# Performance work log

Hardware: AMD Instinct MI355X
Metric: run time of the kernel (lower is better)

## Reference

```python
import jax, jax.numpy as jnp
import numpy as np

B, T, D_IN, D_SAE, K = 256, 8, 768, 8192, 32


def setup_inputs() -> dict:
    key = jax.random.key(0)
    k1, k2, k3 = jax.random.split(key, 3)
    x = jax.random.normal(k1, (B, T, D_IN), dtype=jnp.float32)
    # kaiming_uniform: bound = sqrt(6 / fan_in), fan_in = prod of trailing dims
    bound_e = float(np.sqrt(6.0 / (D_SAE * D_IN)))
    W_enc = jax.random.uniform(k2, (T, D_SAE, D_IN), jnp.float32, -bound_e, bound_e)
    bound_d = float(np.sqrt(6.0 / (D_IN * D_SAE)))
    W_dec = jax.random.uniform(k3, (T, D_IN, D_SAE), jnp.float32, -bound_d, bound_d)
    # decoder column normalization (norm over d_in axis), as in _normalize_decoder
    norms = jnp.clip(jnp.linalg.norm(W_dec, axis=1, keepdims=True), 1e-8)
    W_dec = W_dec / norms
    b_enc = jnp.zeros((T, D_SAE), jnp.float32)
    b_dec = jnp.zeros((T, D_IN), jnp.float32)
    return {"x": x, "W_enc": W_enc, "b_enc": b_enc, "W_dec": W_dec,
            "b_dec": b_dec, "k": K}


def reference(x, W_enc, b_enc, W_dec, b_dec, k):
    # x: (B, T, d_in)
    x_c = x - b_dec[None]                                   # (B, T, d)
    pre = jnp.einsum('btd,thd->bth', x_c, W_enc) + b_enc[None]  # (B, T, h)
    bt = pre.shape[0] * pre.shape[1]
    pre_flat = pre.reshape(bt, -1)
    topk_vals, topk_idx = jax.lax.top_k(pre_flat, k)        # (BT, k)
    rows = jnp.arange(bt)[:, None]
    u_flat = jnp.zeros_like(pre_flat).at[rows, topk_idx].set(jax.nn.relu(topk_vals))
    u = u_flat.reshape(pre.shape)                            # (B, T, h)
    x_hat = jnp.einsum('bth,tdh->btd', u, W_dec) + b_dec[None]
    recon_loss = jnp.mean(jnp.sum((x_hat - x) ** 2, axis=-1))
    return recon_loss, x_hat, u
```

## Files before the change

### kernel.cpp

```cpp
#include <hip/hip_runtime.h>
#include <cstdint>
#include <cstddef>

constexpr int B_SZ  = 256;
constexpr int T_SZ  = 8;
constexpr int DIN   = 768;
constexpr int DSAE  = 8192;
constexpr int KSEL  = 32;
constexpr int NROWS = B_SZ * T_SZ;
constexpr int CAND_CAP = 64;
constexpr int RCAP  = 32;
constexpr float EPS_W = 3.2e-4f;
constexpr int NSK   = DIN / 32;

constexpr size_t XC_SZ    = (size_t)NROWS * DIN;
constexpr size_t OFF_XC   = 0;
constexpr size_t OFF_XCP  = OFF_XC + XC_SZ;
constexpr size_t XCP_W    = XC_SZ / 2;
constexpr size_t OFF_SIDX = OFF_XCP + XCP_W;
constexpr size_t OFF_SVAL = OFF_SIDX + (size_t)NROWS * KSEL;
constexpr size_t OFF_BIG  = OFF_SVAL + (size_t)NROWS * KSEL;
constexpr size_t BIG_W    = (size_t)T_SZ * DSAE * DIN / 2;
constexpr size_t WS_FAST_WORDS = OFF_BIG + BIG_W;

typedef short bf16x8 __attribute__((ext_vector_type(8)));
typedef float f32x4  __attribute__((ext_vector_type(4)));

__device__ inline unsigned rne1(float x) {
  unsigned u = __float_as_uint(x);
  return (u + 0x7FFFu + ((u >> 16) & 1u)) >> 16;
}
__device__ inline float bf16tof(unsigned short v) {
  return __uint_as_float((unsigned)v << 16);
}
__device__ inline unsigned packtr(float a, float b) {
  return (__float_as_uint(a) >> 16) | (__float_as_uint(b) & 0xFFFF0000u);
}

__device__ inline void gload_lds16(const void* g, void* l) {
  __builtin_amdgcn_global_load_lds(
      (const __attribute__((address_space(1))) void*)g,
      (__attribute__((address_space(3))) void*)l, 16, 0, 0);
}

__global__ void k_zero(float* p) { *p = 0.f; }

__global__ __launch_bounds__(256) void k_xc(const float* __restrict__ x,
                                            const float* __restrict__ bdec,
                                            float* __restrict__ xc,
                                            unsigned short* __restrict__ xcp) {
  const int c = blockIdx.x * 256 + threadIdx.x;
  const int lane = c & 63;
  const int u = c >> 6;
  const int s  = u % NSK;
  const int tt = (u / NSK) & (T_SZ - 1);
  const int gm = u / (NSK * T_SZ);
  const int b  = gm * 16 + (lane & 15);
  const int k0 = s * 32 + (lane >> 4) * 8;
  const size_t rowOff = ((size_t)(b * T_SZ + tt)) * DIN + k0;
  float4 v0 = *(const float4*)(x + rowOff);
  float4 v1 = *(const float4*)(x + rowOff + 4);
  float4 d0 = *(const float4*)(bdec + tt * DIN + k0);
  float4 d1 = *(const float4*)(bdec + tt * DIN + k0 + 4);
  v0.x -= d0.x; v0.y -= d0.y; v0.z -= d0.z; v0.w -= d0.w;
  v1.x -= d1.x; v1.y -= d1.y; v1.z -= d1.z; v1.w -= d1.w;
  *(float4*)(xc + rowOff) = v0;
  *(float4*)(xc + rowOff + 4) = v1;
  uint4 p;
  p.x = rne1(v0.x) | (rne1(v0.y) << 16);
  p.y = rne1(v0.z) | (rne1(v0.w) << 16);
  p.z = rne1(v1.x) | (rne1(v1.y) << 16);
  p.w = rne1(v1.z) | (rne1(v1.w) << 16);
  *(uint4*)(xcp + (size_t)c * 8) = p;
}

__global__ __launch_bounds__(256, 2) void k_encoder(const unsigned short* __restrict__ xcp,
                                                    const float* __restrict__ Wenc,
                                                    const float* __restrict__ benc,
                                                    float* __restrict__ pre) {
  __shared__ __align__(16) float Bs[4][64 * 32];
  const int tid = threadIdx.x;
  const int wm = tid >> 6, lane = tid & 63;
  const int l15 = lane & 15, kc = lane >> 4;

  int gRow[2], gCol[2], ldsL[2];
#pragma unroll
  for (int i = 0; i < 2; ++i) {
    int L = i * 4096 + tid * 16;
    int G = L ^ (((L >> 7) & 7) << 4);
    gRow[i] = G >> 7;
    gCol[i] = (G & 127) >> 2;
    ldsL[i] = L;
  }
  int bOff0[4], bOff1[4];
#pragma unroll
  for (int ni = 0; ni < 4; ++ni) {
    int row = ni * 16 + l15;
    int P = row * 128 + kc * 32;
    int sw = (row & 7) << 4;
    bOff0[ni] = P ^ sw;
    bOff1[ni] = (P + 16) ^ sw;
  }
  constexpr size_t A_MI = (size_t)T_SZ * NSK * 512;

  for (int tile = 0; tile < 2; ++tile) {
    const int tileId = blockIdx.x + tile * 512;
    const int t  = tileId >> 7;
    const int n0 = (tileId & 127) * 64;

    const float* bG = Wenc + ((size_t)t * DSAE + n0) * DIN;
    const unsigned short* aP =
        xcp + ((size_t)(wm * 4 * T_SZ + t) * NSK) * 512 + lane * 8;

    auto STAGE = [&](int buf, int s) {
#pragma unroll
      for (int i = 0; i < 2; ++i)
        gload_lds16(bG + (size_t)gRow[i] * DIN + s * 32 + gCol[i],
                    (char*)&Bs[0][0] + buf * 8192 + ldsL[i]);
    };

    f32x4 acc[4][4] = {};
    bf16x8 aA[4], aB[4];

    STAGE(0, 0);
#pragma unroll
    for (int mi = 0; mi < 4; ++mi)
      aA[mi] = *(const bf16x8*)(aP + mi * A_MI);
    STAGE(1, 1);

#define ENC_W6 asm volatile("s_waitcnt vmcnt(6)" ::: "memory")
#define ENC_W4 asm volatile("s_waitcnt vmcnt(4)" ::: "memory")
#define ENC_W0 asm volatile("s_waitcnt vmcnt(0)" ::: "memory")
#define ENC_STEP(u, PFB, PFA, WAITOP) do {                                   \
    if (PFB) STAGE(((u) + 2) & 3, s0 + (u) + 2);                             \
    if (PFA) {                                                               \
      const unsigned short* ap = aP + (size_t)(s0 + (u) + 1) * 512;          \
      _Pragma("unroll")                                                      \
      for (int mi = 0; mi < 4; ++mi) {                                       \
        bf16x8 v = *(const bf16x8*)(ap + mi * A_MI);                         \
        if ((u) % 2 == 0) aB[mi] = v; else aA[mi] = v;                       \
      }                                                                      \
    }                                                                        \
    __builtin_amdgcn_sched_barrier(0);                                       \
    WAITOP;                                                                  \
    __builtin_amdgcn_s_barrier();                                            \
    __builtin_amdgcn_sched_barrier(0);                                       \
    {                                                                        \
      const char* bb = (const char*)&Bs[0][0] + ((u) & 3) * 8192;            \
      _Pragma("unroll")                                                      \
      for (int ni = 0; ni < 4; ++ni) {                                       \
        f32x4 f0 = *(const f32x4*)(bb + bOff0[ni]);                          \
        f32x4 f1 = *(const f32x4*)(bb + bOff1[ni]);                          \
        union { uint32_t w[4]; bf16x8 h; } cvu;                              \
        cvu.w[0] = packtr(f0.x, f0.y); cvu.w[1] = packtr(f0.z, f0.w);        \
        cvu.w[2] = packtr(f1.x, f1.y); cvu.w[3] = packtr(f1.z, f1.w);        \
        _Pragma("unroll")                                                    \
        for (int mi = 0; mi < 4; ++mi)                                       \
          acc[mi][ni] = __builtin_amdgcn_mfma_f32_16x16x32_bf16(             \
              ((u) % 2 == 0) ? aA[mi] : aB[mi], cvu.h, acc[mi][ni], 0, 0, 0);\
      }                                                                      \
    }                                                                        \
  } while (0)

    int s0 = 0;
    for (int g = 0; g < 5; ++g, s0 += 4) {
      ENC_STEP(0, true, true, ENC_W6); ENC_STEP(1, true, true, ENC_W6);
      ENC_STEP(2, true, true, ENC_W6); ENC_STEP(3, true, true, ENC_W6);
    }
    ENC_STEP(0, true, true, ENC_W6);  ENC_STEP(1, true, true, ENC_W6);
    ENC_STEP(2, false, true, ENC_W4); ENC_STEP(3, false, false, ENC_W0);
#undef ENC_STEP
#undef ENC_W6
#undef ENC_W4
#undef ENC_W0

#pragma unroll
    for (int ni = 0; ni < 4; ++ni) {
      const int col = n0 + ni * 16 + l15;
      const float bias = benc[(size_t)t * DSAE + col];
#pragma unroll
      for (int mi = 0; mi < 4; ++mi) {
        const int rbase = wm * 64 + mi * 16 + kc * 4;
#pragma unroll
        for (int j = 0; j < 4; ++j)
          pre[((size_t)(rbase + j) * T_SZ + t) * DSAE + col] = acc[mi][ni][j] + bias;
      }
    }
    if (tile == 0) __syncthreads();
  }
}

__global__ __launch_bounds__(256) void k_select(const float* __restrict__ xc,
                                                const float* __restrict__ Wenc,
                                                const float* __restrict__ benc,
                                                float* u,
                                                int* __restrict__ sel_idx,
                                                float* __restrict__ sel_val) {
  const int r = blockIdx.x, t = r & (T_SZ - 1);
  __shared__ float sp[DSAE];
  __shared__ float redf[4], redf2[4];
  __shared__ int   redi[4];
  __shared__ float cv[CAND_CAP]; __shared__ int ci[CAND_CAP];
  __shared__ float sv[CAND_CAP]; __shared__ int si[CAND_CAP];
  __shared__ float rv[RCAP];     __shared__ int ri[RCAP];
  __shared__ double rd[RCAP];
  __shared__ double xd[DIN];
  __shared__ int   s_n, s_nR, s_A, s_nW;
  const int tid = threadIdx.x, lane = tid & 63, w = tid >> 6;
  float* urow = u + (size_t)r * DSAE;

  float s1 = 0.f, s2 = 0.f;
  for (int sgm = 0; sgm < DSAE / 256; ++sgm) {
    float v = urow[tid + sgm * 256];
    sp[tid + sgm * 256] = v;
    s1 += v; s2 = fmaf(v, v, s2);
  }
  for (int off = 32; off; off >>= 1) {
    s1 += __shfl_down(s1, off); s2 += __shfl_down(s2, off);
  }
  if (lane == 0) { redf[w] = s1; redf2[w] = s2; }
  __syncthreads();
  const float mean = (redf[0] + redf[1] + redf[2] + redf[3]) * (1.f / DSAE);
  const float var  = (redf2[0] + redf2[1] + redf2[2] + redf2[3]) * (1.f / DSAE) - mean * mean;
  const float sd   = sqrtf(fmaxf(var, 1e-20f));

  auto countGE = [&](float th) -> int {
    int c = 0;
#pragma unroll
    for (int sgm = 0; sgm < DSAE / 256; ++sgm)
      c += (sp[tid + sgm * 256] >= th) ? 1 : 0;
    for (int off = 32; off; off >>= 1) c += __shfl_down(c, off);
    __syncthreads();
    if (lane == 0) redi[w] = c;
    __syncthreads();
    return redi[0] + redi[1] + redi[2] + redi[3];
  };

  float tlo = mean + 2.0f * sd, thi = mean + 3.5f * sd;
  for (int it = 0; it < 8 && countGE(tlo) < KSEL; ++it) tlo -= sd;
  float th = mean + 2.52f * sd;
  int c = countGE(th);
  for (int it = 0; it < 24 && (c < KSEL || c > CAND_CAP); ++it) {
    if (c > CAND_CAP) tlo = th; else thi = th;
    th = 0.5f * (tlo + thi);
    c = countGE(th);
  }
  if (c < KSEL) { th = tlo; c = countGE(th); }

  if (tid == 0) s_n = 0;
  __syncthreads();
  for (int sgm = 0; sgm < DSAE / 256; ++sgm) {
    int i = tid + sgm * 256;
    float v = sp[i];
    if (v >= th) {
      int p = atomicAdd(&s_n, 1);
      if (p < CAND_CAP) { cv[p] = v; ci[p] = i; }
    }
  }
  __syncthreads();
  const int n = s_n < CAND_CAP ? s_n : CAND_CAP;

  if (tid < n) {
    float v = cv[tid]; int id = ci[tid];
    int rk = 0;
    for (int j = 0; j < n; ++j) {
      float vj = cv[j];
      rk += (vj > v || (vj == v && ci[j] < id)) ? 1 : 0;
    }
    sv[rk] = v; si[rk] = id;
  }
  __syncthreads();

  const float v32 = sv[KSEL - 1];
  const float wlo = v32 - EPS_W, whi = v32 + EPS_W;
  if (tid == 0) {
    int A = 0;
    while (A < KSEL - 1 && sv[A] > whi) ++A;
    s_A = A;
    int e = A;
    while (e < n && sv[e] >= wlo) ++e;
    s_nW = e - A;
  }
  __syncthreads();
  const int A  = s_A;
  const int nW = s_nW < RCAP ? s_nW : RCAP;
  if (tid < nW) { rv[tid] = sv[A + tid]; ri[tid] = si[A + tid]; }
  if (tid == 0) s_nR = nW;
  __syncthreads();
  if (th > wlo) {
    for (int sgm = 0; sgm < DSAE / 256; ++sgm) {
      int i = tid + sgm * 256;
      float v = sp[i];
      if (v >= wlo && v < th) {
        int p = atomicAdd(&s_nR, 1);
        if (p < RCAP) { rv[p] = v; ri[p] = i; }
      }
    }
  }
  __syncthreads();
  const int nR = s_nR < RCAP ? s_nR : RCAP;

  if (nR >= 2) {
    for (int i = tid; i < DIN; i += 256) xd[i] = (double)xc[(size_t)r * DIN + i];
    __syncthreads();
    for (int j = w; j < nR; j += 4) {
      const int h = ri[j];
      const float* wrow = Wenc + ((size_t)t * DSAE + h) * DIN;
      double s = 0.0;
#pragma unroll
      for (int ss = 0; ss < DIN / 64; ++ss)
        s += xd[lane + 64 * ss] * (double)wrow[lane + 64 * ss];
      for (int off = 32; off; off >>= 1) s += __shfl_down(s, off);
      if (lane == 0) rd[j] = s + (double)benc[(size_t)t * DSAE + h];
    }
  } else if (nR == 1) {
    if (tid == 0) rd[0] = (double)rv[0];
  }
  __syncthreads();

  for (int sgm = 0; sgm < DSAE / 256; ++sgm) urow[tid + sgm * 256] = 0.f;
  __syncthreads();

  if (tid < A) {
    float val = fmaxf(sv[tid], 0.f);
    urow[si[tid]] = val;
    sel_idx[(size_t)r * KSEL + tid] = si[tid];
    sel_val[(size_t)r * KSEL + tid] = val;
  }
  const int need = KSEL - A;
  if (tid < nR) {
    double v = rd[tid]; int id = ri[tid];
    int rk = 0;
    for (int j = 0; j < nR; ++j) {
      double vj = rd[j];
      rk += (vj > v || (vj == v && ri[j] < id)) ? 1 : 0;
    }
    if (rk < need) {
      float val = fmaxf((float)v, 0.f);
      urow[id] = val;
      sel_idx[(size_t)r * KSEL + A + rk] = id;
      sel_val[(size_t)r * KSEL + A + rk] = val;
    }
  }
}

__global__ __launch_bounds__(256) void k_transpose(const float* __restrict__ W,
                                                   unsigned short* __restrict__ Wt) {
  __shared__ float s[32][33];
  const int t  = blockIdx.z;
  const int h0 = blockIdx.x * 32;
  const int d0 = blockIdx.y * 32;
  const int c  = threadIdx.x & 31, rr = threadIdx.x >> 5;
#pragma unroll
  for (int q = 0; q < 4; ++q) {
    int d = d0 + rr + q * 8;
    s[rr + q * 8][c] = W[((size_t)t * DIN + d) * DSAE + h0 + c];
  }
  __syncthreads();
#pragma unroll
  for (int q = 0; q < 4; ++q) {
    int h = h0 + rr + q * 8;
    Wt[((size_t)t * DSAE + h) * DIN + d0 + c] = (unsigned short)rne1(s[c][rr + q * 8]);
  }
}

template <bool TRANSPOSED>
__global__ __launch_bounds__(256) void k_decoder(const void* __restrict__ Wd_,
                                                 const float* __restrict__ x,
                                                 const float* __restrict__ bdec,
                                                 const int* __restrict__ sel_idx,
                                                 const float* __restrict__ sel_val,
                                                 float* __restrict__ xhat,
                                                 float* __restrict__ loss) {
  const int r = blockIdx.x, t = r & (T_SZ - 1);
  __shared__ int   si[KSEL];
  __shared__ float sv[KSEL];
  __shared__ float rbuf[4];
  const int tid = threadIdx.x;
  if (tid < KSEL) {
    si[tid] = sel_idx[(size_t)r * KSEL + tid] & (DSAE - 1);
    sv[tid] = sel_val[(size_t)r * KSEL + tid];
  }
  __syncthreads();

  float acc[3];
#pragma unroll
  for (int i = 0; i < 3; ++i) acc[i] = bdec[(size_t)t * DIN + tid + 256 * i];
#pragma unroll 4
  for (int j = 0; j < KSEL; ++j) {
    const int h = si[j];
    const float v = sv[j];
    if (TRANSPOSED) {
      const unsigned short* wrow =
          (const unsigned short*)Wd_ + ((size_t)t * DSAE + h) * DIN;
#pragma unroll
      for (int i = 0; i < 3; ++i)
        acc[i] = fmaf(v, bf16tof(wrow[tid + 256 * i]), acc[i]);
    } else {
      const float* Wd = (const float*)Wd_;
#pragma unroll
      for (int i = 0; i < 3; ++i)
        acc[i] = fmaf(v, Wd[((size_t)t * DIN + tid + 256 * i) * DSAE + h], acc[i]);
    }
  }
  float sq = 0.f;
#pragma unroll
  for (int i = 0; i < 3; ++i) {
    const int d = tid + 256 * i;
    const float xv = x[(size_t)r * DIN + d];
    xhat[(size_t)r * DIN + d] = acc[i];
    const float e = acc[i] - xv;
    sq = fmaf(e, e, sq);
  }
  for (int off = 32; off; off >>= 1) sq += __shfl_down(sq, off);
  if ((tid & 63) == 0) rbuf[tid >> 6] = sq;
  __syncthreads();
  if (tid == 0)
    atomicAdd(loss, (rbuf[0] + rbuf[1] + rbuf[2] + rbuf[3]) * (1.0f / NROWS));
}

extern "C" void kernel_launch(void* const* d_in, const int* in_sizes, int n_in,
                              void* d_out, int out_size, void* d_ws, size_t ws_size,
                              hipStream_t stream) {
  const float* x    = (const float*)d_in[0];
  const float* Wenc = (const float*)d_in[1];
  const float* benc = (const float*)d_in[2];
  const float* Wdec = (const float*)d_in[3];
  const float* bdec = (const float*)d_in[4];

  float* out  = (float*)d_out;
  float* loss = out;
  float* xhat = out + 1;
  float* u    = out + 1 + (size_t)NROWS * DIN;

  float*          wsf  = (float*)d_ws;
  float*          xc   = wsf + OFF_XC;
  unsigned short* xcp  = (unsigned short*)(wsf + OFF_XCP);
  int*            sidx = (int*)(wsf + OFF_SIDX);
  float*          sval = wsf + OFF_SVAL;
  unsigned short* big  = (unsigned short*)(wsf + OFF_BIG);
  const bool fast = ws_size >= WS_FAST_WORDS * sizeof(float);

  k_zero<<<1, 1, 0, stream>>>(loss);
  k_xc<<<NROWS * DIN / (256 * 8), 256, 0, stream>>>(x, bdec, xc, xcp);
  k_encoder<<<512, 256, 0, stream>>>(xcp, Wenc, benc, u);
  k_select<<<NROWS, 256, 0, stream>>>(xc, Wenc, benc, u, sidx, sval);
  if (fast) {
    k_transpose<<<dim3(DSAE / 32, DIN / 32, T_SZ), 256, 0, stream>>>(Wdec, big);
    k_decoder<true><<<NROWS, 256, 0, stream>>>(big, x, bdec, sidx, sval, xhat, loss);
  } else {
    k_decoder<false><<<NROWS, 256, 0, stream>>>(Wdec, x, bdec, sidx, sval, xhat, loss);
  }
}
```

Before: 240.2 us.

## Fuse top-k candidate capture into encoder and decode directly from untransposed weights

A new kernel computes a per-row threshold proportional to the norm of the centred input. The encoder epilogue then appends every pre-activation above that threshold to a per-row candidate list using global atomics. The selection kernel uses this list when it holds enough candidates and the boundary window stays above the threshold, and falls back to the full-row scan otherwise. The separate transpose-to-bf16 pass and row-wise decoder are replaced by a decoder with one block per (d, t). Each block stages one fp32 weight row of 8192 entries in shared memory and gathers the selected entries for all batch rows, which removes the extra transpose write and read. The threshold constant is tuned to the weight scale, so the fast path depends on the input statistics; the encoder also gains atomic contention in its epilogue.

```diff
diff --git a/kernel.cpp b/kernel.cpp
--- a/kernel.cpp
+++ b/kernel.cpp
@@ -9,9 +9,11 @@
 constexpr int KSEL  = 32;
 constexpr int NROWS = B_SZ * T_SZ;
 constexpr int CAND_CAP = 64;
+constexpr int CFCAP = 128;
 constexpr int RCAP  = 32;
 constexpr float EPS_W = 3.2e-4f;
 constexpr int NSK   = DIN / 32;
+constexpr float TAU_C = 1.324943e-3f;
 
 constexpr size_t XC_SZ    = (size_t)NROWS * DIN;
 constexpr size_t OFF_XC   = 0;
@@ -19,9 +21,11 @@
 constexpr size_t XCP_W    = XC_SZ / 2;
 constexpr size_t OFF_SIDX = OFF_XCP + XCP_W;
 constexpr size_t OFF_SVAL = OFF_SIDX + (size_t)NROWS * KSEL;
-constexpr size_t OFF_BIG  = OFF_SVAL + (size_t)NROWS * KSEL;
-constexpr size_t BIG_W    = (size_t)T_SZ * DSAE * DIN / 2;
-constexpr size_t WS_FAST_WORDS = OFF_BIG + BIG_W;
+constexpr size_t OFF_TAU  = OFF_SVAL + (size_t)NROWS * KSEL;
+constexpr size_t OFF_CCNT = OFF_TAU + NROWS;
+constexpr size_t OFF_CIDX = OFF_CCNT + NROWS;
+constexpr size_t OFF_CVAL = OFF_CIDX + (size_t)NROWS * CFCAP;
+constexpr size_t WS_WORDS = OFF_CVAL + (size_t)NROWS * CFCAP;
 
 typedef short bf16x8 __attribute__((ext_vector_type(8)));
 typedef float f32x4  __attribute__((ext_vector_type(4)));
@@ -30,20 +34,14 @@
   unsigned u = __float_as_uint(x);
   return (u + 0x7FFFu + ((u >> 16) & 1u)) >> 16;
 }
-__device__ inline float bf16tof(unsigned short v) {
-  return __uint_as_float((unsigned)v << 16);
-}
 __device__ inline unsigned packtr(float a, float b) {
   return (__float_as_uint(a) >> 16) | (__float_as_uint(b) & 0xFFFF0000u);
 }
-
 __device__ inline void gload_lds16(const void* g, void* l) {
   __builtin_amdgcn_global_load_lds(
       (const __attribute__((address_space(1))) void*)g,
       (__attribute__((address_space(3))) void*)l, 16, 0, 0);
 }
-
-__global__ void k_zero(float* p) { *p = 0.f; }
 
 __global__ __launch_bounds__(256) void k_xc(const float* __restrict__ x,
                                             const float* __restrict__ bdec,
@@ -74,10 +72,32 @@
   *(uint4*)(xcp + (size_t)c * 8) = p;
 }
 
+__global__ __launch_bounds__(256) void k_tau(const float* __restrict__ xc,
+                                             float* __restrict__ tau,
+                                             int* __restrict__ ccnt,
+                                             float* __restrict__ loss) {
+  const int tid = threadIdx.x, lane = tid & 63, w = tid >> 6;
+  if (blockIdx.x < 8) ccnt[blockIdx.x * 256 + tid] = 0;
+  if (blockIdx.x == 0 && tid == 0) *loss = 0.f;
+  const int r = blockIdx.x * 4 + w;
+  float s = 0.f;
+#pragma unroll
+  for (int ld = 0; ld < 3; ++ld) {
+    float4 v = *(const float4*)(xc + (size_t)r * DIN + ld * 256 + lane * 4);
+    s = fmaf(v.x, v.x, fmaf(v.y, v.y, fmaf(v.z, v.z, fmaf(v.w, v.w, s))));
+  }
+  for (int off = 32; off; off >>= 1) s += __shfl_down(s, off);
+  if (lane == 0) tau[r] = TAU_C * sqrtf(s);
+}
+
 __global__ __launch_bounds__(256, 2) void k_encoder(const unsigned short* __restrict__ xcp,
                                                     const float* __restrict__ Wenc,
                                                     const float* __restrict__ benc,
-                                                    float* __restrict__ pre) {
+                                                    float* __restrict__ pre,
+                                                    const float* __restrict__ tau,
+                                                    int* __restrict__ ccnt,
+                                                    int* __restrict__ cidx,
+                                                    float* __restrict__ cval) {
   __shared__ __align__(16) float Bs[4][64 * 32];
   const int tid = threadIdx.x;
   const int wm = tid >> 6, lane = tid & 63;
@@ -121,7 +141,6 @@
 
     f32x4 acc[4][4] = {};
     bf16x8 aA[4], aB[4];
-
     STAGE(0, 0);
 #pragma unroll
     for (int mi = 0; mi < 4; ++mi)
@@ -174,6 +193,13 @@
 #undef ENC_W4
 #undef ENC_W0
 
+    float tv[4][4];
+#pragma unroll
+    for (int mi = 0; mi < 4; ++mi)
+#pragma unroll
+      for (int j = 0; j < 4; ++j)
+        tv[mi][j] = tau[(wm * 64 + mi * 16 + kc * 4 + j) * T_SZ + t];
+
 #pragma unroll
     for (int ni = 0; ni < 4; ++ni) {
       const int col = n0 + ni * 16 + l15;
@@ -182,8 +208,18 @@
       for (int mi = 0; mi < 4; ++mi) {
         const int rbase = wm * 64 + mi * 16 + kc * 4;
 #pragma unroll
-        for (int j = 0; j < 4; ++j)
-          pre[((size_t)(rbase + j) * T_SZ + t) * DSAE + col] = acc[mi][ni][j] + bias;
+        for (int j = 0; j < 4; ++j) {
+          const float v = acc[mi][ni][j] + bias;
+          const int rr = (rbase + j) * T_SZ + t;
+          pre[(size_t)rr * DSAE + col] = v;
+          if (v >= tv[mi][j]) {
+            int pos = atomicAdd(&ccnt[rr], 1);
+            if (pos < CFCAP) {
+              cidx[(size_t)rr * CFCAP + pos] = col;
+              cval[(size_t)rr * CFCAP + pos] = v;
+            }
+          }
+        }
       }
     }
     if (tile == 0) __syncthreads();
@@ -195,99 +231,125 @@
                                                 const float* __restrict__ benc,
                                                 float* u,
                                                 int* __restrict__ sel_idx,
-                                                float* __restrict__ sel_val) {
+                                                float* __restrict__ sel_val,
+                                                const float* __restrict__ tau,
+                                                const int* __restrict__ ccnt,
+                                                const int* __restrict__ cidx,
+                                                const float* __restrict__ cval) {
   const int r = blockIdx.x, t = r & (T_SZ - 1);
   __shared__ float sp[DSAE];
   __shared__ float redf[4], redf2[4];
   __shared__ int   redi[4];
-  __shared__ float cv[CAND_CAP]; __shared__ int ci[CAND_CAP];
-  __shared__ float sv[CAND_CAP]; __shared__ int si[CAND_CAP];
-  __shared__ float rv[RCAP];     __shared__ int ri[RCAP];
+  __shared__ float cv[CFCAP]; __shared__ int ci[CFCAP];
+  __shared__ float sv[CFCAP]; __shared__ int si[CFCAP];
+  __shared__ float rv[RCAP];  __shared__ int ri[RCAP];
   __shared__ double rd[RCAP];
   __shared__ double xd[DIN];
-  __shared__ int   s_n, s_nR, s_A, s_nW;
+  __shared__ int s_n, s_nR, s_A, s_nW;
   const int tid = threadIdx.x, lane = tid & 63, w = tid >> 6;
   float* urow = u + (size_t)r * DSAE;
 
-  float s1 = 0.f, s2 = 0.f;
-  for (int sgm = 0; sgm < DSAE / 256; ++sgm) {
-    float v = urow[tid + sgm * 256];
-    sp[tid + sgm * 256] = v;
-    s1 += v; s2 = fmaf(v, v, s2);
-  }
-  for (int off = 32; off; off >>= 1) {
-    s1 += __shfl_down(s1, off); s2 += __shfl_down(s2, off);
-  }
-  if (lane == 0) { redf[w] = s1; redf2[w] = s2; }
-  __syncthreads();
-  const float mean = (redf[0] + redf[1] + redf[2] + redf[3]) * (1.f / DSAE);
-  const float var  = (redf2[0] + redf2[1] + redf2[2] + redf2[3]) * (1.f / DSAE) - mean * mean;
-  const float sd   = sqrtf(fmaxf(var, 1e-20f));
-
-  auto countGE = [&](float th) -> int {
-    int c = 0;
-#pragma unroll
-    for (int sgm = 0; sgm < DSAE / 256; ++sgm)
-      c += (sp[tid + sgm * 256] >= th) ? 1 : 0;
-    for (int off = 32; off; off >>= 1) c += __shfl_down(c, off);
+  const int cnt = ccnt[r];
+  const float taur = tau[r];
+  bool tryFast = (cnt >= KSEL && cnt <= CFCAP);
+  bool usedFast = false;
+  float th = taur;
+  int n = 0;
+  float v32, wlo, whi;
+
+  for (;;) {
+    usedFast = tryFast;
     __syncthreads();
-    if (lane == 0) redi[w] = c;
+    if (tryFast) {
+      n = cnt;
+      th = taur;
+      for (int i = tid; i < cnt; i += 256) {
+        cv[i] = cval[(size_t)r * CFCAP + i];
+        ci[i] = cidx[(size_t)r * CFCAP + i];
+      }
+    } else {
+      float s1 = 0.f, s2 = 0.f;
+      for (int sgm = 0; sgm < DSAE / 256; ++sgm) {
+        float v = urow[tid + sgm * 256];
+        sp[tid + sgm * 256] = v;
+        s1 += v; s2 = fmaf(v, v, s2);
+      }
+      for (int off = 32; off; off >>= 1) {
+        s1 += __shfl_down(s1, off); s2 += __shfl_down(s2, off);
+      }
+      if (lane == 0) { redf[w] = s1; redf2[w] = s2; }
+      __syncthreads();
+      const float mean = (redf[0] + redf[1] + redf[2] + redf[3]) * (1.f / DSAE);
+      const float var  = (redf2[0] + redf2[1] + redf2[2] + redf2[3]) * (1.f / DSAE) - mean * mean;
+      const float sd   = sqrtf(fmaxf(var, 1e-20f));
+      auto countGE = [&](float thv) -> int {
+        int c = 0;
+#pragma unroll
+        for (int sgm = 0; sgm < DSAE / 256; ++sgm)
+          c += (sp[tid + sgm * 256] >= thv) ? 1 : 0;
+        for (int off = 32; off; off >>= 1) c += __shfl_down(c, off);
+        __syncthreads();
+        if (lane == 0) redi[w] = c;
+        __syncthreads();
+        return redi[0] + redi[1] + redi[2] + redi[3];
+      };
+      float tlo = mean + 2.0f * sd, thi2 = mean + 3.5f * sd;
+      for (int it = 0; it < 8 && countGE(tlo) < KSEL; ++it) tlo -= sd;
+      th = mean + 2.52f * sd;
+      int c = countGE(th);
+      for (int it = 0; it < 24 && (c < KSEL || c > CAND_CAP); ++it) {
+        if (c > CAND_CAP) tlo = th; else thi2 = th;
+        th = 0.5f * (tlo + thi2);
+        c = countGE(th);
+      }
+      if (c < KSEL) { th = tlo; c = countGE(th); }
+      if (tid == 0) s_n = 0;
+      __syncthreads();
+      for (int sgm = 0; sgm < DSAE / 256; ++sgm) {
+        int i = tid + sgm * 256;
+        float v = sp[i];
+        if (v >= th) {
+          int p = atomicAdd(&s_n, 1);
+          if (p < CAND_CAP) { cv[p] = v; ci[p] = i; }
+        }
+      }
+      __syncthreads();
+      n = s_n < CAND_CAP ? s_n : CAND_CAP;
+    }
     __syncthreads();
-    return redi[0] + redi[1] + redi[2] + redi[3];
-  };
-
-  float tlo = mean + 2.0f * sd, thi = mean + 3.5f * sd;
-  for (int it = 0; it < 8 && countGE(tlo) < KSEL; ++it) tlo -= sd;
-  float th = mean + 2.52f * sd;
-  int c = countGE(th);
-  for (int it = 0; it < 24 && (c < KSEL || c > CAND_CAP); ++it) {
-    if (c > CAND_CAP) tlo = th; else thi = th;
-    th = 0.5f * (tlo + thi);
-    c = countGE(th);
-  }
-  if (c < KSEL) { th = tlo; c = countGE(th); }
-
-  if (tid == 0) s_n = 0;
-  __syncthreads();
-  for (int sgm = 0; sgm < DSAE / 256; ++sgm) {
-    int i = tid + sgm * 256;
-    float v = sp[i];
-    if (v >= th) {
-      int p = atomicAdd(&s_n, 1);
-      if (p < CAND_CAP) { cv[p] = v; ci[p] = i; }
-    }
-  }
-  __syncthreads();
-  const int n = s_n < CAND_CAP ? s_n : CAND_CAP;
-
-  if (tid < n) {
-    float v = cv[tid]; int id = ci[tid];
-    int rk = 0;
-    for (int j = 0; j < n; ++j) {
-      float vj = cv[j];
-      rk += (vj > v || (vj == v && ci[j] < id)) ? 1 : 0;
-    }
-    sv[rk] = v; si[rk] = id;
-  }
-  __syncthreads();
-
-  const float v32 = sv[KSEL - 1];
-  const float wlo = v32 - EPS_W, whi = v32 + EPS_W;
-  if (tid == 0) {
-    int A = 0;
-    while (A < KSEL - 1 && sv[A] > whi) ++A;
-    s_A = A;
-    int e = A;
-    while (e < n && sv[e] >= wlo) ++e;
-    s_nW = e - A;
-  }
-  __syncthreads();
+
+    if (tid < n) {
+      float v = cv[tid]; int id = ci[tid];
+      int rk = 0;
+      for (int j = 0; j < n; ++j) {
+        float vj = cv[j];
+        rk += (vj > v || (vj == v && ci[j] < id)) ? 1 : 0;
+      }
+      sv[rk] = v; si[rk] = id;
+    }
+    __syncthreads();
+
+    v32 = sv[KSEL - 1];
+    wlo = v32 - EPS_W; whi = v32 + EPS_W;
+    if (tid == 0) {
+      int A = 0;
+      while (A < KSEL - 1 && sv[A] > whi) ++A;
+      s_A = A;
+      int e = A;
+      while (e < n && sv[e] >= wlo) ++e;
+      s_nW = e - A;
+    }
+    __syncthreads();
+    if (usedFast && (wlo <= taur || s_nW > RCAP)) { tryFast = false; continue; }
+    break;
+  }
+
   const int A  = s_A;
   const int nW = s_nW < RCAP ? s_nW : RCAP;
   if (tid < nW) { rv[tid] = sv[A + tid]; ri[tid] = si[A + tid]; }
   if (tid == 0) s_nR = nW;
   __syncthreads();
-  if (th > wlo) {
+  if (!usedFast && th > wlo) {
     for (int sgm = 0; sgm < DSAE / 256; ++sgm) {
       int i = tid + sgm * 256;
       float v = sp[i];
@@ -344,74 +406,33 @@
   }
 }
 
-__global__ __launch_bounds__(256) void k_transpose(const float* __restrict__ W,
-                                                   unsigned short* __restrict__ Wt) {
-  __shared__ float s[32][33];
-  const int t  = blockIdx.z;
-  const int h0 = blockIdx.x * 32;
-  const int d0 = blockIdx.y * 32;
-  const int c  = threadIdx.x & 31, rr = threadIdx.x >> 5;
-#pragma unroll
-  for (int q = 0; q < 4; ++q) {
-    int d = d0 + rr + q * 8;
-    s[rr + q * 8][c] = W[((size_t)t * DIN + d) * DSAE + h0 + c];
-  }
-  __syncthreads();
-#pragma unroll
-  for (int q = 0; q < 4; ++q) {
-    int h = h0 + rr + q * 8;
-    Wt[((size_t)t * DSAE + h) * DIN + d0 + c] = (unsigned short)rne1(s[c][rr + q * 8]);
-  }
-}
-
-template <bool TRANSPOSED>
-__global__ __launch_bounds__(256) void k_decoder(const void* __restrict__ Wd_,
-                                                 const float* __restrict__ x,
-                                                 const float* __restrict__ bdec,
-                                                 const int* __restrict__ sel_idx,
-                                                 const float* __restrict__ sel_val,
-                                                 float* __restrict__ xhat,
-                                                 float* __restrict__ loss) {
-  const int r = blockIdx.x, t = r & (T_SZ - 1);
-  __shared__ int   si[KSEL];
-  __shared__ float sv[KSEL];
+__global__ __launch_bounds__(256) void k_dec_direct(const float* __restrict__ Wdec,
+                                                    const float* __restrict__ x,
+                                                    const float* __restrict__ bdec,
+                                                    const int* __restrict__ sel_idx,
+                                                    const float* __restrict__ sel_val,
+                                                    float* __restrict__ xhat,
+                                                    float* __restrict__ loss) {
+  __shared__ float row[DSAE];
   __shared__ float rbuf[4];
+  const int d = blockIdx.x, t = blockIdx.y;
   const int tid = threadIdx.x;
-  if (tid < KSEL) {
-    si[tid] = sel_idx[(size_t)r * KSEL + tid] & (DSAE - 1);
-    sv[tid] = sel_val[(size_t)r * KSEL + tid];
-  }
-  __syncthreads();
-
-  float acc[3];
-#pragma unroll
-  for (int i = 0; i < 3; ++i) acc[i] = bdec[(size_t)t * DIN + tid + 256 * i];
-#pragma unroll 4
+  const float* src = Wdec + ((size_t)t * DIN + d) * DSAE;
+#pragma unroll
+  for (int i = 0; i < 8; ++i)
+    *(float4*)&row[i * 1024 + tid * 4] = *(const float4*)(src + i * 1024 + tid * 4);
+  __syncthreads();
+
+  const int r = tid * T_SZ + t;
+  float acc = bdec[(size_t)t * DIN + d];
+#pragma unroll 8
   for (int j = 0; j < KSEL; ++j) {
-    const int h = si[j];
-    const float v = sv[j];
-    if (TRANSPOSED) {
-      const unsigned short* wrow =
-          (const unsigned short*)Wd_ + ((size_t)t * DSAE + h) * DIN;
-#pragma unroll
-      for (int i = 0; i < 3; ++i)
-        acc[i] = fmaf(v, bf16tof(wrow[tid + 256 * i]), acc[i]);
-    } else {
-      const float* Wd = (const float*)Wd_;
-#pragma unroll
-      for (int i = 0; i < 3; ++i)
-        acc[i] = fmaf(v, Wd[((size_t)t * DIN + tid + 256 * i) * DSAE + h], acc[i]);
-    }
-  }
-  float sq = 0.f;
-#pragma unroll
-  for (int i = 0; i < 3; ++i) {
-    const int d = tid + 256 * i;
-    const float xv = x[(size_t)r * DIN + d];
-    xhat[(size_t)r * DIN + d] = acc[i];
-    const float e = acc[i] - xv;
-    sq = fmaf(e, e, sq);
-  }
+    const int h = sel_idx[(size_t)r * KSEL + j] & (DSAE - 1);
+    acc = fmaf(sel_val[(size_t)r * KSEL + j], row[h], acc);
+  }
+  xhat[(size_t)r * DIN + d] = acc;
+  const float e = acc - x[(size_t)r * DIN + d];
+  float sq = e * e;
   for (int off = 32; off; off >>= 1) sq += __shfl_down(sq, off);
   if ((tid & 63) == 0) rbuf[tid >> 6] = sq;
   __syncthreads();
@@ -438,17 +459,16 @@
   unsigned short* xcp  = (unsigned short*)(wsf + OFF_XCP);
   int*            sidx = (int*)(wsf + OFF_SIDX);
   float*          sval = wsf + OFF_SVAL;
-  unsigned short* big  = (unsigned short*)(wsf + OFF_BIG);
-  const bool fast = ws_size >= WS_FAST_WORDS * sizeof(float);
-
-  k_zero<<<1, 1, 0, stream>>>(loss);
+  float*          tau  = wsf + OFF_TAU;
+  int*            ccnt = (int*)(wsf + OFF_CCNT);
+  int*            cidx = (int*)(wsf + OFF_CIDX);
+  float*          cval = wsf + OFF_CVAL;
+
   k_xc<<<NROWS * DIN / (256 * 8), 256, 0, stream>>>(x, bdec, xc, xcp);
-  k_encoder<<<512, 256, 0, stream>>>(xcp, Wenc, benc, u);
-  k_select<<<NROWS, 256, 0, stream>>>(xc, Wenc, benc, u, sidx, sval);
-  if (fast) {
-    k_transpose<<<dim3(DSAE / 32, DIN / 32, T_SZ), 256, 0, stream>>>(Wdec, big);
-    k_decoder<true><<<NROWS, 256, 0, stream>>>(big, x, bdec, sidx, sval, xhat, loss);
-  } else {
-    k_decoder<false><<<NROWS, 256, 0, stream>>>(Wdec, x, bdec, sidx, sval, xhat, loss);
-  }
-}
+  k_tau<<<NROWS / 4, 256, 0, stream>>>(xc, tau, ccnt, loss);
+  k_encoder<<<512, 256, 0, stream>>>(xcp, Wenc, benc, u, tau, ccnt, cidx, cval);
+  k_select<<<NROWS, 256, 0, stream>>>(xc, Wenc, benc, u, sidx, sval,
+                                      tau, ccnt, cidx, cval);
+  k_dec_direct<<<dim3(DIN, T_SZ), 256, 0, stream>>>(Wdec, x, bdec, sidx, sval,
+                                                    xhat, loss);
+}
```

Measured after the change: 276.9 us. 1.15x slower.

## Replace decoder transpose with per-(d,t) LDS-staged row gather decoder

Applied to the files above, without the earlier changes.

Removes the full bf16 transpose of W_dec and the row-gather decoder. Each block now streams one contiguous W_dec row (all hidden units for a given output dim and timestep) into shared memory, and each thread gathers its batch row's 32 selected weights from LDS. W_dec is read once, coalesced, in fp32, avoiding the transpose's extra read/write traffic. The cost is strided reads of selection indices/values per thread and more atomic loss adds.

```diff
diff --git a/kernel.cpp b/kernel.cpp
--- a/kernel.cpp
+++ b/kernel.cpp
@@ -19,9 +19,7 @@
 constexpr size_t XCP_W    = XC_SZ / 2;
 constexpr size_t OFF_SIDX = OFF_XCP + XCP_W;
 constexpr size_t OFF_SVAL = OFF_SIDX + (size_t)NROWS * KSEL;
-constexpr size_t OFF_BIG  = OFF_SVAL + (size_t)NROWS * KSEL;
-constexpr size_t BIG_W    = (size_t)T_SZ * DSAE * DIN / 2;
-constexpr size_t WS_FAST_WORDS = OFF_BIG + BIG_W;
+constexpr size_t WS_WORDS = OFF_SVAL + (size_t)NROWS * KSEL;
 
 typedef short bf16x8 __attribute__((ext_vector_type(8)));
 typedef float f32x4  __attribute__((ext_vector_type(4)));
@@ -30,13 +28,9 @@
   unsigned u = __float_as_uint(x);
   return (u + 0x7FFFu + ((u >> 16) & 1u)) >> 16;
 }
-__device__ inline float bf16tof(unsigned short v) {
-  return __uint_as_float((unsigned)v << 16);
-}
 __device__ inline unsigned packtr(float a, float b) {
   return (__float_as_uint(a) >> 16) | (__float_as_uint(b) & 0xFFFF0000u);
 }
-
 __device__ inline void gload_lds16(const void* g, void* l) {
   __builtin_amdgcn_global_load_lds(
       (const __attribute__((address_space(1))) void*)g,
@@ -121,7 +115,6 @@
 
     f32x4 acc[4][4] = {};
     bf16x8 aA[4], aB[4];
-
     STAGE(0, 0);
 #pragma unroll
     for (int mi = 0; mi < 4; ++mi)
@@ -344,74 +337,33 @@
   }
 }
 
-__global__ __launch_bounds__(256) void k_transpose(const float* __restrict__ W,
-                                                   unsigned short* __restrict__ Wt) {
-  __shared__ float s[32][33];
-  const int t  = blockIdx.z;
-  const int h0 = blockIdx.x * 32;
-  const int d0 = blockIdx.y * 32;
-  const int c  = threadIdx.x & 31, rr = threadIdx.x >> 5;
-#pragma unroll
-  for (int q = 0; q < 4; ++q) {
-    int d = d0 + rr + q * 8;
-    s[rr + q * 8][c] = W[((size_t)t * DIN + d) * DSAE + h0 + c];
-  }
-  __syncthreads();
-#pragma unroll
-  for (int q = 0; q < 4; ++q) {
-    int h = h0 + rr + q * 8;
-    Wt[((size_t)t * DSAE + h) * DIN + d0 + c] = (unsigned short)rne1(s[c][rr + q * 8]);
-  }
-}
-
-template <bool TRANSPOSED>
-__global__ __launch_bounds__(256) void k_decoder(const void* __restrict__ Wd_,
-                                                 const float* __restrict__ x,
-                                                 const float* __restrict__ bdec,
-                                                 const int* __restrict__ sel_idx,
-                                                 const float* __restrict__ sel_val,
-                                                 float* __restrict__ xhat,
-                                                 float* __restrict__ loss) {
-  const int r = blockIdx.x, t = r & (T_SZ - 1);
-  __shared__ int   si[KSEL];
-  __shared__ float sv[KSEL];
+__global__ __launch_bounds__(256) void k_dec_direct(const float* __restrict__ Wdec,
+                                                    const float* __restrict__ x,
+                                                    const float* __restrict__ bdec,
+                                                    const int* __restrict__ sel_idx,
+                                                    const float* __restrict__ sel_val,
+                                                    float* __restrict__ xhat,
+                                                    float* __restrict__ loss) {
+  __shared__ float row[DSAE];
   __shared__ float rbuf[4];
+  const int d = blockIdx.x, t = blockIdx.y;
   const int tid = threadIdx.x;
-  if (tid < KSEL) {
-    si[tid] = sel_idx[(size_t)r * KSEL + tid] & (DSAE - 1);
-    sv[tid] = sel_val[(size_t)r * KSEL + tid];
-  }
-  __syncthreads();
-
-  float acc[3];
-#pragma unroll
-  for (int i = 0; i < 3; ++i) acc[i] = bdec[(size_t)t * DIN + tid + 256 * i];
-#pragma unroll 4
+  const float* src = Wdec + ((size_t)t * DIN + d) * DSAE;
+#pragma unroll
+  for (int i = 0; i < 8; ++i)
+    *(float4*)&row[i * 1024 + tid * 4] = *(const float4*)(src + i * 1024 + tid * 4);
+  __syncthreads();
+
+  const int r = tid * T_SZ + t;
+  float acc = bdec[(size_t)t * DIN + d];
+#pragma unroll 8
   for (int j = 0; j < KSEL; ++j) {
-    const int h = si[j];
-    const float v = sv[j];
-    if (TRANSPOSED) {
-      const unsigned short* wrow =
-          (const unsigned short*)Wd_ + ((size_t)t * DSAE + h) * DIN;
-#pragma unroll
-      for (int i = 0; i < 3; ++i)
-        acc[i] = fmaf(v, bf16tof(wrow[tid + 256 * i]), acc[i]);
-    } else {
-      const float* Wd = (const float*)Wd_;
-#pragma unroll
-      for (int i = 0; i < 3; ++i)
-        acc[i] = fmaf(v, Wd[((size_t)t * DIN + tid + 256 * i) * DSAE + h], acc[i]);
-    }
-  }
-  float sq = 0.f;
-#pragma unroll
-  for (int i = 0; i < 3; ++i) {
-    const int d = tid + 256 * i;
-    const float xv = x[(size_t)r * DIN + d];
-    xhat[(size_t)r * DIN + d] = acc[i];
-    const float e = acc[i] - xv;
-    sq = fmaf(e, e, sq);
-  }
+    const int h = sel_idx[(size_t)r * KSEL + j] & (DSAE - 1);
+    acc = fmaf(sel_val[(size_t)r * KSEL + j], row[h], acc);
+  }
+  xhat[(size_t)r * DIN + d] = acc;
+  const float e = acc - x[(size_t)r * DIN + d];
+  float sq = e * e;
   for (int off = 32; off; off >>= 1) sq += __shfl_down(sq, off);
   if ((tid & 63) == 0) rbuf[tid >> 6] = sq;
   __syncthreads();
@@ -438,17 +390,11 @@
   unsigned short* xcp  = (unsigned short*)(wsf + OFF_XCP);
   int*            sidx = (int*)(wsf + OFF_SIDX);
   float*          sval = wsf + OFF_SVAL;
-  unsigned short* big  = (unsigned short*)(wsf + OFF_BIG);
-  const bool fast = ws_size >= WS_FAST_WORDS * sizeof(float);
 
   k_zero<<<1, 1, 0, stream>>>(loss);
   k_xc<<<NROWS * DIN / (256 * 8), 256, 0, stream>>>(x, bdec, xc, xcp);
   k_encoder<<<512, 256, 0, stream>>>(xcp, Wenc, benc, u);
   k_select<<<NROWS, 256, 0, stream>>>(xc, Wenc, benc, u, sidx, sval);
-  if (fast) {
-    k_transpose<<<dim3(DSAE / 32, DIN / 32, T_SZ), 256, 0, stream>>>(Wdec, big);
-    k_decoder<true><<<NROWS, 256, 0, stream>>>(big, x, bdec, sidx, sval, xhat, loss);
-  } else {
-    k_decoder<false><<<NROWS, 256, 0, stream>>>(Wdec, x, bdec, sidx, sval, xhat, loss);
-  }
-}
+  k_dec_direct<<<dim3(DIN, T_SZ), 256, 0, stream>>>(Wdec, x, bdec, sidx, sval,
+                                                    xhat, loss);
+}
```

Result: slower. 256.4 us (+6.7%).
